# Optimization experiments

Hardware: AMD Instinct MI355X
Metric: run time of the kernel (lower is better)

Reference implementation:

```python
import jax, jax.numpy as jnp
import numpy as np

N, E, G = 20000, 100000, 32
HID, HEADS, HC = 64, 8, 64  # hidden, heads, per-head channels (PyG: out_channels per head)
L, K = 3, 4


def setup_inputs() -> dict:
    key = jax.random.key(0)
    ks = jax.random.split(key, 20)
    rn = lambda k, s, sc=0.05: jax.random.normal(k, s, jnp.float32) * sc
    HO = HEADS * HC  # 512
    return {
        "x": jax.random.uniform(ks[0], (N, 7), jnp.float32),
        "edge_attr": jax.random.normal(ks[1], (E, 4), jnp.float32),
        "means": jax.random.normal(ks[2], (K, 8), jnp.float32),
        "log_stds": jnp.zeros((K, 8), jnp.float32),
        "sp_W": rn(ks[3], (K, HID), 0.3), "sp_b": jnp.zeros((HID,), jnp.float32),
        "ne_W": rn(ks[4], (7, HID), 0.3), "ne_b": jnp.zeros((HID,), jnp.float32),
        "ee_W": rn(ks[5], (4, HID), 0.3), "ee_b": jnp.zeros((HID,), jnp.float32),
        "Wq": rn(ks[6], (L, HID, HO)), "bq": jnp.zeros((L, HO), jnp.float32),
        "Wk": rn(ks[7], (L, HID, HO)), "bk": jnp.zeros((L, HO), jnp.float32),
        "Wv": rn(ks[8], (L, HID, HO)), "bv": jnp.zeros((L, HO), jnp.float32),
        "We": rn(ks[9], (L, HID, HO)), "be": jnp.zeros((L, HO), jnp.float32),
        "Ws": rn(ks[10], (L, HID, HID)), "bs": jnp.zeros((L, HID), jnp.float32),
        "eu_W": rn(ks[11], (L, 3 * HID, HID)), "eu_b": jnp.zeros((L, HID), jnp.float32),
        "rW1": rn(ks[12], (2 * HID, HID)), "rb1": jnp.zeros((HID,), jnp.float32),
        "rW2": rn(ks[13], (HID, HID)), "rb2": jnp.zeros((HID,), jnp.float32),
        "rW3": rn(ks[14], (HID, 2)), "rb3": jnp.zeros((2,), jnp.float32),
        "edge_index": jax.random.randint(ks[15], (2, E), 0, N, jnp.int32),
        "batch": jnp.sort(jax.random.randint(ks[16], (N,), 0, G, jnp.int32)),
        "num_graphs": G,
    }


def reference(x, edge_attr, means, log_stds, sp_W, sp_b, ne_W, ne_b, ee_W, ee_b,
              Wq, bq, Wk, bk, Wv, bv, We, be, Ws, bs, eu_W, eu_b,
              rW1, rb1, rW2, rb2, rW3, rb3, edge_index, batch, num_graphs):
    n = x.shape[0]
    src, dst = edge_index[0], edge_index[1]

    # ---- SpatialGaussianEncoder (dropout is identity in eval) ----
    p = x[:, :4]
    sl, sr = p[src, :2], p[src, 2:4]
    dl, dr = p[dst, :2], p[dst, 2:4]
    rel = jnp.stack([dl - sl, dl - sr, dr - sl, dr - sr], axis=1)  # [E,4,2]
    dist = jnp.linalg.norm(rel, axis=-1)                           # [E,4]
    ang = jnp.arctan2(rel[..., 1], rel[..., 0])                    # [E,4]
    u = jnp.stack([dist, ang], axis=-1).reshape(-1, 8)             # [E,8] (d,a)x4
    std = jnp.exp(log_stds) + 1e-6                                 # [K,8]
    z = (u[:, None, :] - means[None]) / std[None]                  # [E,K,8]
    w = jnp.exp(-0.5 * jnp.sum(z * z, axis=-1))                    # [E,K]
    sp = jax.nn.relu(w @ sp_W + sp_b)                              # [E,HID]

    h = jax.nn.relu(x @ ne_W + ne_b)                               # [N,HID]
    ea = jax.nn.relu(edge_attr @ ee_W + ee_b) + sp                 # [E,HID]

    scale = 1.0 / float(np.sqrt(HC))
    for l in range(L):
        # PyG TransformerConv(hidden, hidden, heads=8, edge_dim=hidden, concat=False)
        q = (h @ Wq[l] + bq[l]).reshape(n, HEADS, HC)
        k = (h @ Wk[l] + bk[l]).reshape(n, HEADS, HC)
        v = (h @ Wv[l] + bv[l]).reshape(n, HEADS, HC)
        e = (ea @ We[l] + be[l]).reshape(-1, HEADS, HC)
        kj = k[src] + e                                            # [E,H,C]
        alpha = jnp.einsum('ehc,ehc->eh', q[dst], kj) * scale      # [E,H]
        m = jax.ops.segment_max(alpha, dst, num_segments=n)
        ex = jnp.exp(alpha - m[dst])
        den = jax.ops.segment_sum(ex, dst, num_segments=n)
        a = ex / (den[dst] + 1e-16)                                # scatter-softmax over dst
        msg = a[:, :, None] * (v[src] + e)                         # [E,H,C]
        out = jax.ops.segment_sum(msg, dst, num_segments=n).mean(axis=1)  # concat=False -> head mean
        h = jax.nn.relu(out + h @ Ws[l] + bs[l])                   # skip (root_weight) + F.relu
        ef = jnp.concatenate([h[src], h[dst], ea], axis=1)         # [E,3*HID]
        ea = jax.nn.relu(ef @ eu_W[l] + eu_b[l])

    # ---- per-graph masked-mean pooling == segment mean ----
    cn = jnp.maximum(jax.ops.segment_sum(jnp.ones((n,), x.dtype), batch, num_segments=num_graphs), 1.0)
    node_pool = jax.ops.segment_sum(h, batch, num_segments=num_graphs) / cn[:, None]
    eb = batch[src]
    ce = jnp.maximum(jax.ops.segment_sum(jnp.ones((src.shape[0],), x.dtype), eb, num_segments=num_graphs), 1.0)
    edge_pool = jax.ops.segment_sum(ea, eb, num_segments=num_graphs) / ce[:, None]
    g = jnp.concatenate([node_pool, edge_pool], axis=1)            # [G,2*HID]

    h1 = jax.nn.relu(g @ rW1 + rb1)
    h2 = jax.nn.relu(h1 @ rW2 + rb2)
    return jnp.tanh(h2 @ rW3 + rb3)                                # [G,2]
```

## Files before the change

### kernel.cpp

```cpp
#include <hip/hip_runtime.h>
#include <hip/hip_bf16.h>
#include <cstdint>
#include <cstddef>



__global__ void __launch_bounds__(256) k_node_embed(
    const float* __restrict__ x, const float* __restrict__ neW, const float* __restrict__ neb,
    float* __restrict__ h, int N)
{
    int idx = blockIdx.x * 256 + threadIdx.x;
    int n = idx >> 6, c = idx & 63;
    if (n >= N) return;
    float acc = neb[c];
    #pragma unroll
    for (int j = 0; j < 7; ++j) acc += x[(size_t)n * 7 + j] * neW[j * 64 + c];
    h[(size_t)n * 64 + c] = fmaxf(acc, 0.f);
}

__global__ void __launch_bounds__(256) k_edge_w(
    const float* __restrict__ x,
    const float* __restrict__ means, const float* __restrict__ log_stds,
    const int* __restrict__ src, const int* __restrict__ dst,
    float* __restrict__ wbuf, int E)
{
    int e = blockIdx.x * 256 + threadIdx.x;
    if (e >= E) return;
    int s = src[e], d = dst[e];
    const float* ps = x + (size_t)s * 7;
    const float* pd = x + (size_t)d * 7;
    float slx = ps[0], sly = ps[1], srx = ps[2], sry = ps[3];
    float dlx = pd[0], dly = pd[1], drx = pd[2], dry = pd[3];
    float u[8];
    float rx, ry;
    rx = dlx - slx; ry = dly - sly; u[0] = sqrtf(rx*rx + ry*ry); u[1] = atan2f(ry, rx);
    rx = dlx - srx; ry = dly - sry; u[2] = sqrtf(rx*rx + ry*ry); u[3] = atan2f(ry, rx);
    rx = drx - slx; ry = dry - sly; u[4] = sqrtf(rx*rx + ry*ry); u[5] = atan2f(ry, rx);
    rx = drx - srx; ry = dry - sry; u[6] = sqrtf(rx*rx + ry*ry); u[7] = atan2f(ry, rx);
    #pragma unroll
    for (int kk = 0; kk < 4; ++kk) {
        float ssum = 0.f;
        #pragma unroll
        for (int dd = 0; dd < 8; ++dd) {
            float stdv = expf(log_stds[kk*8+dd]) + 1e-6f;
            float z = (u[dd] - means[kk*8+dd]) / stdv;
            ssum += z * z;
        }
        wbuf[(size_t)e*4 + kk] = expf(-0.5f * ssum);
    }
}

__global__ void __launch_bounds__(256) k_edge_ea(
    const float* __restrict__ edge_attr, const float* __restrict__ wbuf,
    const float* __restrict__ spW, const float* __restrict__ spb,
    const float* __restrict__ eeW, const float* __restrict__ eeb,
    float* __restrict__ ea, int E)
{
    int idx = blockIdx.x * 256 + threadIdx.x;
    int e = idx >> 6, c = idx & 63;
    if (e >= E) return;
    float acce = eeb[c];
    #pragma unroll
    for (int j = 0; j < 4; ++j) acce += edge_attr[(size_t)e*4 + j] * eeW[j*64 + c];
    float accs = spb[c];
    #pragma unroll
    for (int j = 0; j < 4; ++j) accs += wbuf[(size_t)e*4 + j] * spW[j*64 + c];
    ea[(size_t)e*64 + c] = fmaxf(acce, 0.f) + fmaxf(accs, 0.f);
}


__global__ void __launch_bounds__(256) k_hist(
    const int* __restrict__ dst, int* __restrict__ deg, int E)
{
    int e = blockIdx.x * 256 + threadIdx.x;
    if (e < E) atomicAdd(deg + dst[e], 1);
}

__global__ void __launch_bounds__(1024) k_scan(
    const int* __restrict__ deg, int* __restrict__ ptr, int* __restrict__ headw, int N)
{
    __shared__ int part[1024];
    int t = threadIdx.x;
    int per = (N + 1023) / 1024;
    int s = 0;
    for (int i = 0; i < per; ++i) { int idx = t*per + i; if (idx < N) s += deg[idx]; }
    part[t] = s;
    __syncthreads();
    for (int off = 1; off < 1024; off <<= 1) {
        int v = (t >= off) ? part[t - off] : 0;
        __syncthreads();
        part[t] += v;
        __syncthreads();
    }
    int base = (t > 0) ? part[t - 1] : 0;
    for (int i = 0; i < per; ++i) {
        int idx = t*per + i;
        if (idx < N) { ptr[idx] = base; headw[idx] = base; base += deg[idx]; }
    }
    if (t == 1023) ptr[N] = part[1023];
}

__global__ void __launch_bounds__(256) k_scatter(
    const int* __restrict__ dst, const int* __restrict__ src, const int* __restrict__ batch,
    int* __restrict__ headw, int2* __restrict__ ipair, int* __restrict__ ieb, int E)
{
    int e = blockIdx.x * 256 + threadIdx.x;
    if (e < E) {
        int s = src[e];
        int pos = atomicAdd(headw + dst[e], 1);
        ipair[pos] = make_int2(s, e);
        ieb[e] = batch[s];
    }
}


__global__ void __launch_bounds__(256) k_wprod_all(
    const float* __restrict__ Wq, const float* __restrict__ bq,
    const float* __restrict__ Wk, const float* __restrict__ We,
    float* __restrict__ Mk, float* __restrict__ Me,
    float* __restrict__ bqk, float* __restrict__ bqe)
{
    int h = blockIdx.x;
    int which = blockIdx.y;
    int l = blockIdx.z;
    const float* Wq_l = Wq + (size_t)l * 64 * 512;
    const float* bq_l = bq + (size_t)l * 512;
    const float* Wx_l = (which ? We : Wk) + (size_t)l * 64 * 512;
    float* M  = (which ? Me : Mk) + (size_t)l * 64 * 512;
    float* bM = (which ? bqe : bqk) + (size_t)l * 512;
    __shared__ float wq_s[65][64];
    __shared__ float wx_s[64][65];
    int tid = threadIdx.x;
    for (int i = tid; i < 4096; i += 256) {
        int r = i >> 6, c2 = i & 63;
        wq_s[r][c2] = Wq_l[(size_t)r*512 + h*64 + c2];
        wx_s[r][c2] = Wx_l[(size_t)r*512 + h*64 + c2];
    }
    if (tid < 64) wq_s[64][tid] = bq_l[h*64 + tid];
    __syncthreads();
    int j = tid & 63, cg = tid >> 6;
    for (int c = cg*16; c < cg*16 + 16; ++c) {
        float s = 0.f;
        #pragma unroll 8
        for (int c2 = 0; c2 < 64; ++c2) s += wq_s[c][c2] * wx_s[j][c2];
        M[(size_t)c*512 + h*64 + j] = s;
    }
    if (tid < 64) {
        float s = 0.f;
        #pragma unroll 8
        for (int c2 = 0; c2 < 64; ++c2) s += wq_s[64][c2] * wx_s[tid][c2];
        bM[h*64 + tid] = s;
    }
}

__global__ void __launch_bounds__(64) k_wqb_all(
    const float* __restrict__ Wq, const float* __restrict__ bq,
    const float* __restrict__ bk, const float* __restrict__ be,
    float* __restrict__ wqb, float* __restrict__ cb)
{
    int l = blockIdx.x;
    const float* Wq_l = Wq + (size_t)l * 64 * 512;
    const float* bq_l = bq + (size_t)l * 512;
    const float* bk_l = bk + (size_t)l * 512;
    const float* be_l = be + (size_t)l * 512;
    float* wqb_l = wqb + (size_t)l * 512;
    float* cb_l  = cb + (size_t)l * 8;
    int c = threadIdx.x;
    for (int h = 0; h < 8; ++h) {
        float s = 0.f;
        for (int c2 = 0; c2 < 64; ++c2)
            s += Wq_l[(size_t)c*512 + h*64 + c2] * (bk_l[h*64+c2] + be_l[h*64+c2]);
        wqb_l[c*8 + h] = s;
    }
    if (c < 8) {
        float s = 0.f;
        for (int c2 = 0; c2 < 64; ++c2)
            s += bq_l[c*64 + c2] * (bk_l[c*64+c2] + be_l[c*64+c2]);
        cb_l[c] = s;
    }
}


__global__ void __launch_bounds__(256) k_proj16(
    const float* __restrict__ h,
    const float* __restrict__ Mk, const float* __restrict__ bqk, float* __restrict__ qk,
    const float* __restrict__ Me, const float* __restrict__ bqe, float* __restrict__ qe2,
    int N)
{
    __shared__ float As[64][132];
    __shared__ __align__(16) float Wt[64][64];
    int tid = threadIdx.x;
    int y = blockIdx.y;
    int which = y >> 3, yb = y & 7;
    const float* W    = which ? Me : Mk;
    const float* bias = (which ? bqe : bqk) + yb * 64;
    float* Y          = which ? qe2 : qk;
    int n0 = blockIdx.x * 128;
    {
        int rt = tid & 127;
        int n = n0 + rt;
        int jh = (tid >> 7) * 32;
        if (n < N) {
            const float* ap = h + (size_t)n*64;
            #pragma unroll
            for (int j4 = 0; j4 < 8; ++j4) {
                int j = jh + j4 * 4;
                float4 a = *(const float4*)(ap + j);
                As[j+0][rt] = a.x; As[j+1][rt] = a.y;
                As[j+2][rt] = a.z; As[j+3][rt] = a.w;
            }
        } else {
            #pragma unroll
            for (int j4 = 0; j4 < 8; ++j4) {
                int j = jh + j4 * 4;
                As[j+0][rt] = 0.f; As[j+1][rt] = 0.f;
                As[j+2][rt] = 0.f; As[j+3][rt] = 0.f;
            }
        }
        #pragma unroll
        for (int i = 0; i < 4; ++i) {
            int idx = tid + i * 256;
            int j = idx >> 4, c4 = (idx & 15) * 4;
            *(float4*)&Wt[j][c4] = *(const float4*)(W + (size_t)j*512 + yb*64 + c4);
        }
    }
    __syncthreads();
    int wv = tid >> 6, lane = tid & 63;
    int rg = lane >> 3, cg = lane & 7;
    int c0 = cg * 8;
    int rbase = wv * 32 + rg * 4;
    float acc[4][8];
    float4 b0 = *(const float4*)(bias + c0);
    float4 b1 = *(const float4*)(bias + c0 + 4);
    #pragma unroll
    for (int t = 0; t < 4; ++t) {
        acc[t][0]=b0.x; acc[t][1]=b0.y; acc[t][2]=b0.z; acc[t][3]=b0.w;
        acc[t][4]=b1.x; acc[t][5]=b1.y; acc[t][6]=b1.z; acc[t][7]=b1.w;
    }
    #pragma unroll 4
    for (int j = 0; j < 64; ++j) {
        float4 av = *(const float4*)&As[j][rbase];
        float4 w0 = *(const float4*)&Wt[j][c0];
        float4 w1 = *(const float4*)&Wt[j][c0 + 4];
        acc[0][0] += av.x*w0.x; acc[0][1] += av.x*w0.y; acc[0][2] += av.x*w0.z; acc[0][3] += av.x*w0.w;
        acc[0][4] += av.x*w1.x; acc[0][5] += av.x*w1.y; acc[0][6] += av.x*w1.z; acc[0][7] += av.x*w1.w;
        acc[1][0] += av.y*w0.x; acc[1][1] += av.y*w0.y; acc[1][2] += av.y*w0.z; acc[1][3] += av.y*w0.w;
        acc[1][4] += av.y*w1.x; acc[1][5] += av.y*w1.y; acc[1][6] += av.y*w1.z; acc[1][7] += av.y*w1.w;
        acc[2][0] += av.z*w0.x; acc[2][1] += av.z*w0.y; acc[2][2] += av.z*w0.z; acc[2][3] += av.z*w0.w;
        acc[2][4] += av.z*w1.x; acc[2][5] += av.z*w1.y; acc[2][6] += av.z*w1.z; acc[2][7] += av.z*w1.w;
        acc[3][0] += av.w*w0.x; acc[3][1] += av.w*w0.y; acc[3][2] += av.w*w0.z; acc[3][3] += av.w*w0.w;
        acc[3][4] += av.w*w1.x; acc[3][5] += av.w*w1.y; acc[3][6] += av.w*w1.z; acc[3][7] += av.w*w1.w;
    }
    #pragma unroll
    for (int t = 0; t < 4; ++t) {
        int n = n0 + rbase + t;
        if (n < N) {
            float4 o0 = {acc[t][0],acc[t][1],acc[t][2],acc[t][3]};
            float4 o1 = {acc[t][4],acc[t][5],acc[t][6],acc[t][7]};
            *(float4*)(Y + (size_t)n*512 + yb*64 + c0)     = o0;
            *(float4*)(Y + (size_t)n*512 + yb*64 + c0 + 4) = o1;
        }
    }
}


__global__ void __launch_bounds__(256) k_attn_fused(
    const float* __restrict__ qk, const float* __restrict__ qe2,
    const float* __restrict__ wqb, const float* __restrict__ cb,
    const float* __restrict__ ea, const float* __restrict__ hbuf,
    const int* __restrict__ ptr, const int2* __restrict__ ipair,
    float* __restrict__ hagg, float* __restrict__ tbuf, float* __restrict__ sbuf, int N)
{
    int wv = threadIdx.x >> 6, lane = threadIdx.x & 63;
    int n = blockIdx.x * 4 + wv;
    if (n >= N) return;
    int h = lane >> 3, p = lane & 7;
    int b = ptr[n], e_ = ptr[n + 1];
    int deg = e_ - b;
    const float4* xp = (const float4*)(qk + (size_t)n*512 + lane*8);
    float4 x0 = xp[0], x1 = xp[1];
    const float4* gp = (const float4*)(qe2 + (size_t)n*512 + lane*8);
    float4 g0 = gp[0], g1 = gp[1];
    const float4* hdp = (const float4*)(hbuf + (size_t)n*64 + p*8);
    float4 hd0 = hdp[0], hd1 = hdp[1];
    float qbh = hd0.x*wqb[(p*8+0)*8+h] + hd0.y*wqb[(p*8+1)*8+h]
              + hd0.z*wqb[(p*8+2)*8+h] + hd0.w*wqb[(p*8+3)*8+h]
              + hd1.x*wqb[(p*8+4)*8+h] + hd1.y*wqb[(p*8+5)*8+h]
              + hd1.z*wqb[(p*8+6)*8+h] + hd1.w*wqb[(p*8+7)*8+h];
    qbh += __shfl_xor(qbh, 1);
    qbh += __shfl_xor(qbh, 2);
    qbh += __shfl_xor(qbh, 4);
    qbh += cb[h];
    float m = -3.4e38f, den = 0.f;
    float hacc[8], tacc[8];
    #pragma unroll
    for (int i = 0; i < 8; ++i) { hacc[i] = 0.f; tacc[i] = 0.f; }
    for (int base = 0; base < deg; base += 64) {
        int cnt = deg - base; if (cnt > 64) cnt = 64;
        int2 myp = (lane < cnt) ? ipair[b + base + lane] : make_int2(0, 0);
        int s0i = __shfl(myp.x, 0), e0i = __shfl(myp.y, 0);
        const float4* hp = (const float4*)(hbuf + (size_t)s0i*64 + p*8);
        const float4* ap = (const float4*)(ea + (size_t)e0i*64 + p*8);
        float4 h0 = hp[0], h1 = hp[1];
        float4 a0 = ap[0], a1 = ap[1];
        for (int i = 0; i < cnt; ++i) {
            float4 h0c = h0, h1c = h1, a0c = a0, a1c = a1;
            if (i + 1 < cnt) {
                int sn = __shfl(myp.x, i + 1), en = __shfl(myp.y, i + 1);
                const float4* hpn = (const float4*)(hbuf + (size_t)sn*64 + p*8);
                const float4* apn = (const float4*)(ea + (size_t)en*64 + p*8);
                h0 = hpn[0]; h1 = hpn[1]; a0 = apn[0]; a1 = apn[1];
            }
            float t = x0.x*h0c.x + x0.y*h0c.y + x0.z*h0c.z + x0.w*h0c.w
                    + x1.x*h1c.x + x1.y*h1c.y + x1.z*h1c.z + x1.w*h1c.w
                    + g0.x*a0c.x + g0.y*a0c.y + g0.z*a0c.z + g0.w*a0c.w
                    + g1.x*a1c.x + g1.y*a1c.y + g1.z*a1c.z + g1.w*a1c.w;
            t += __shfl_xor(t, 1);
            t += __shfl_xor(t, 2);
            t += __shfl_xor(t, 4);
            float al = 0.125f * (t + qbh);
            float mn = fmaxf(m, al);
            float r = expf(m - mn);
            float w = expf(al - mn);
            den = den * r + w;
            m = mn;
            hacc[0] = hacc[0]*r + w*h0c.x; hacc[1] = hacc[1]*r + w*h0c.y;
            hacc[2] = hacc[2]*r + w*h0c.z; hacc[3] = hacc[3]*r + w*h0c.w;
            hacc[4] = hacc[4]*r + w*h1c.x; hacc[5] = hacc[5]*r + w*h1c.y;
            hacc[6] = hacc[6]*r + w*h1c.z; hacc[7] = hacc[7]*r + w*h1c.w;
            tacc[0] = tacc[0]*r + w*a0c.x; tacc[1] = tacc[1]*r + w*a0c.y;
            tacc[2] = tacc[2]*r + w*a0c.z; tacc[3] = tacc[3]*r + w*a0c.w;
            tacc[4] = tacc[4]*r + w*a1c.x; tacc[5] = tacc[5]*r + w*a1c.y;
            tacc[6] = tacc[6]*r + w*a1c.z; tacc[7] = tacc[7]*r + w*a1c.w;
        }
    }
    float inv = 0.125f / (den + 1e-16f);
    float4 o;
    o = {hacc[0]*inv,hacc[1]*inv,hacc[2]*inv,hacc[3]*inv};
    *(float4*)(hagg + (size_t)n*512 + lane*8)     = o;
    o = {hacc[4]*inv,hacc[5]*inv,hacc[6]*inv,hacc[7]*inv};
    *(float4*)(hagg + (size_t)n*512 + lane*8 + 4) = o;
    o = {tacc[0]*inv,tacc[1]*inv,tacc[2]*inv,tacc[3]*inv};
    *(float4*)(tbuf + (size_t)n*512 + lane*8)     = o;
    o = {tacc[4]*inv,tacc[5]*inv,tacc[6]*inv,tacc[7]*inv};
    *(float4*)(tbuf + (size_t)n*512 + lane*8 + 4) = o;
    if (p == 0) sbuf[(size_t)n*8 + h] = den * inv;
}

__global__ void __launch_bounds__(256) k_nf_gemm2(
    const float* __restrict__ tbuf, const float* __restrict__ hagg,
    const float* __restrict__ We, const float* __restrict__ Wv,
    float* __restrict__ pbuf, int N)
{
    __shared__ float As[64][132];
    __shared__ __align__(16) float Wt[64][64];
    int tid = threadIdx.x;
    int g = blockIdx.y;
    int n0 = blockIdx.x * 128;
    int wv = tid >> 6, lane = tid & 63;
    int rg = lane >> 3, cg = lane & 7;
    int c0 = cg * 8;
    int rbase = wv * 32 + rg * 4;
    float acc[4][8];
    #pragma unroll
    for (int t = 0; t < 4; ++t)
        #pragma unroll
        for (int i = 0; i < 8; ++i) acc[t][i] = 0.f;
    #pragma unroll
    for (int yy = 0; yy < 2; ++yy) {
        int y = g * 2 + yy;
        #pragma unroll
        for (int round = 0; round < 2; ++round) {
            const float* A = round ? hagg : tbuf;
            const float* W = round ? Wv : We;
            {
                int rt = tid & 127;
                int n = n0 + rt;
                int jh = (tid >> 7) * 32;
                if (n < N) {
                    const float* ap = A + (size_t)n*512 + y*64;
                    #pragma unroll
                    for (int j4 = 0; j4 < 8; ++j4) {
                        int j = jh + j4 * 4;
                        float4 a = *(const float4*)(ap + j);
                        As[j+0][rt] = a.x; As[j+1][rt] = a.y;
                        As[j+2][rt] = a.z; As[j+3][rt] = a.w;
                    }
                } else {
                    #pragma unroll
                    for (int j4 = 0; j4 < 8; ++j4) {
                        int j = jh + j4 * 4;
                        As[j+0][rt] = 0.f; As[j+1][rt] = 0.f;
                        As[j+2][rt] = 0.f; As[j+3][rt] = 0.f;
                    }
                }
                #pragma unroll
                for (int i = 0; i < 4; ++i) {
                    int idx = tid + i * 256;
                    int j = idx >> 4, c4 = (idx & 15) * 4;
                    *(float4*)&Wt[j][c4] = *(const float4*)(W + (size_t)j*512 + y*64 + c4);
                }
            }
            __syncthreads();
            #pragma unroll 4
            for (int j = 0; j < 64; ++j) {
                float4 av = *(const float4*)&As[j][rbase];
                float4 w0 = *(const float4*)&Wt[j][c0];
                float4 w1 = *(const float4*)&Wt[j][c0 + 4];
                acc[0][0] += av.x*w0.x; acc[0][1] += av.x*w0.y; acc[0][2] += av.x*w0.z; acc[0][3] += av.x*w0.w;
                acc[0][4] += av.x*w1.x; acc[0][5] += av.x*w1.y; acc[0][6] += av.x*w1.z; acc[0][7] += av.x*w1.w;
                acc[1][0] += av.y*w0.x; acc[1][1] += av.y*w0.y; acc[1][2] += av.y*w0.z; acc[1][3] += av.y*w0.w;
                acc[1][4] += av.y*w1.x; acc[1][5] += av.y*w1.y; acc[1][6] += av.y*w1.z; acc[1][7] += av.y*w1.w;
                acc[2][0] += av.z*w0.x; acc[2][1] += av.z*w0.y; acc[2][2] += av.z*w0.z; acc[2][3] += av.z*w0.w;
                acc[2][4] += av.z*w1.x; acc[2][5] += av.z*w1.y; acc[2][6] += av.z*w1.z; acc[2][7] += av.z*w1.w;
                acc[3][0] += av.w*w0.x; acc[3][1] += av.w*w0.y; acc[3][2] += av.w*w0.z; acc[3][3] += av.w*w0.w;
                acc[3][4] += av.w*w1.x; acc[3][5] += av.w*w1.y; acc[3][6] += av.w*w1.z; acc[3][7] += av.w*w1.w;
            }
            __syncthreads();
        }
    }
    float* out = pbuf + (size_t)g * N * 64;
    #pragma unroll
    for (int t = 0; t < 4; ++t) {
        int n = n0 + rbase + t;
        if (n < N) {
            float4 o0 = {acc[t][0],acc[t][1],acc[t][2],acc[t][3]};
            float4 o1 = {acc[t][4],acc[t][5],acc[t][6],acc[t][7]};
            *(float4*)(out + (size_t)n*64 + c0)     = o0;
            *(float4*)(out + (size_t)n*64 + c0 + 4) = o1;
        }
    }
}

__global__ void __launch_bounds__(256) k_nf_reduce2(
    const float* __restrict__ pbuf, const float* __restrict__ hin,
    const float* __restrict__ sbuf, const float* __restrict__ Ws,
    const float* __restrict__ be, const float* __restrict__ bv,
    const float* __restrict__ bs, float* __restrict__ hnext, int N)
{
    int idx = blockIdx.x * 256 + threadIdx.x;
    int n = idx >> 6, cc = idx & 63;
    if (n >= N) return;
    float a = bs[cc];
    #pragma unroll
    for (int y = 0; y < 4; ++y) a += pbuf[(size_t)y*N*64 + (size_t)n*64 + cc];
    float hv = hin[(size_t)n*64 + cc];
    #pragma unroll 8
    for (int j = 0; j < 64; ++j) a += __shfl(hv, j) * Ws[(size_t)j*64 + cc];
    #pragma unroll
    for (int h = 0; h < 8; ++h)
        a += sbuf[(size_t)n*8 + h] * (be[h*64 + cc] + bv[h*64 + cc]);
    hnext[(size_t)n*64 + cc] = fmaxf(a, 0.f);
}

__global__ void __launch_bounds__(256) k_eu_pre(
    const float* __restrict__ h, const float* __restrict__ euW,
    float* __restrict__ hw, int N)
{
    __shared__ float As[64][132];
    __shared__ __align__(16) float Wt[64][64];
    int tid = threadIdx.x;
    int y = blockIdx.y;
    int n0 = blockIdx.x * 128;
    {
        int rt = tid & 127;
        int n = n0 + rt;
        int jh = (tid >> 7) * 32;
        if (n < N) {
            const float* ap = h + (size_t)n*64;
            #pragma unroll
            for (int j4 = 0; j4 < 8; ++j4) {
                int j = jh + j4 * 4;
                float4 a = *(const float4*)(ap + j);
                As[j+0][rt] = a.x; As[j+1][rt] = a.y;
                As[j+2][rt] = a.z; As[j+3][rt] = a.w;
            }
        } else {
            #pragma unroll
            for (int j4 = 0; j4 < 8; ++j4) {
                int j = jh + j4 * 4;
                As[j+0][rt] = 0.f; As[j+1][rt] = 0.f;
                As[j+2][rt] = 0.f; As[j+3][rt] = 0.f;
            }
        }
        #pragma unroll
        for (int i = 0; i < 4; ++i) {
            int idx = tid + i * 256;
            *(float4*)&Wt[idx >> 4][(idx & 15) * 4] =
                *(const float4*)(euW + (size_t)y*4096 + idx * 4);
        }
    }
    __syncthreads();
    int wv = tid >> 6, lane = tid & 63;
    int rg = lane >> 3, cg = lane & 7;
    int c0 = cg * 8;
    int rbase = wv * 32 + rg * 4;
    float acc[4][8];
    #pragma unroll
    for (int t = 0; t < 4; ++t)
        #pragma unroll
        for (int i = 0; i < 8; ++i) acc[t][i] = 0.f;
    #pragma unroll 4
    for (int j = 0; j < 64; ++j) {
        float4 av = *(const float4*)&As[j][rbase];
        float4 w0 = *(const float4*)&Wt[j][c0];
        float4 w1 = *(const float4*)&Wt[j][c0 + 4];
        acc[0][0] += av.x*w0.x; acc[0][1] += av.x*w0.y; acc[0][2] += av.x*w0.z; acc[0][3] += av.x*w0.w;
        acc[0][4] += av.x*w1.x; acc[0][5] += av.x*w1.y; acc[0][6] += av.x*w1.z; acc[0][7] += av.x*w1.w;
        acc[1][0] += av.y*w0.x; acc[1][1] += av.y*w0.y; acc[1][2] += av.y*w0.z; acc[1][3] += av.y*w0.w;
        acc[1][4] += av.y*w1.x; acc[1][5] += av.y*w1.y; acc[1][6] += av.y*w1.z; acc[1][7] += av.y*w1.w;
        acc[2][0] += av.z*w0.x; acc[2][1] += av.z*w0.y; acc[2][2] += av.z*w0.z; acc[2][3] += av.z*w0.w;
        acc[2][4] += av.z*w1.x; acc[2][5] += av.z*w1.y; acc[2][6] += av.z*w1.z; acc[2][7] += av.z*w1.w;
        acc[3][0] += av.w*w0.x; acc[3][1] += av.w*w0.y; acc[3][2] += av.w*w0.z; acc[3][3] += av.w*w0.w;
        acc[3][4] += av.w*w1.x; acc[3][5] += av.w*w1.y; acc[3][6] += av.w*w1.z; acc[3][7] += av.w*w1.w;
    }
    #pragma unroll
    for (int t = 0; t < 4; ++t) {
        int n = n0 + rbase + t;
        if (n < N) {
            float4 o0 = {acc[t][0],acc[t][1],acc[t][2],acc[t][3]};
            float4 o1 = {acc[t][4],acc[t][5],acc[t][6],acc[t][7]};
            *(float4*)(hw + (size_t)n*128 + y*64 + c0)     = o0;
            *(float4*)(hw + (size_t)n*128 + y*64 + c0 + 4) = o1;
        }
    }
}

__global__ void __launch_bounds__(256) k_edge_update2(
    const float* __restrict__ hw, const float* __restrict__ ea,
    const float* __restrict__ euW2, const float* __restrict__ eub,
    const int* __restrict__ src, const int* __restrict__ dst,
    float* __restrict__ ea2, int E)
{
    __shared__ float As[64][132];
    __shared__ __align__(16) float Wt[64][64];
    __shared__ int sid[128], did[128];
    int tid = threadIdx.x;
    int e0 = blockIdx.x * 128;
    if (tid < 128) {
        int e = e0 + tid; if (e >= E) e = E - 1;
        sid[tid] = src[e]; did[tid] = dst[e];
    }
    {
        int et = tid & 127;
        int e = e0 + et; if (e >= E) e = E - 1;
        const float* ap = ea + (size_t)e * 64;
        int jh = (tid >> 7) * 32;
        #pragma unroll
        for (int j4 = 0; j4 < 8; ++j4) {
            int j = jh + j4 * 4;
            float4 a = *(const float4*)(ap + j);
            As[j+0][et] = a.x; As[j+1][et] = a.y;
            As[j+2][et] = a.z; As[j+3][et] = a.w;
        }
        #pragma unroll
        for (int i = 0; i < 4; ++i) {
            int idx = tid + i * 256;
            *(float4*)&Wt[idx >> 4][(idx & 15) * 4] = *(const float4*)(euW2 + idx * 4);
        }
    }
    __syncthreads();
    int wv = tid >> 6, lane = tid & 63;
    int rg = lane >> 3, cg = lane & 7;
    int c0 = cg * 8;
    int rbase = wv * 32 + rg * 4;
    float acc[4][8];
    float4 b0 = *(const float4*)(eub + c0);
    float4 b1 = *(const float4*)(eub + c0 + 4);
    #pragma unroll
    for (int t = 0; t < 4; ++t) {
        acc[t][0]=b0.x; acc[t][1]=b0.y; acc[t][2]=b0.z; acc[t][3]=b0.w;
        acc[t][4]=b1.x; acc[t][5]=b1.y; acc[t][6]=b1.z; acc[t][7]=b1.w;
    }
    #pragma unroll 4
    for (int j = 0; j < 64; ++j) {
        float4 av = *(const float4*)&As[j][rbase];
        float4 w0 = *(const float4*)&Wt[j][c0];
        float4 w1 = *(const float4*)&Wt[j][c0 + 4];
        acc[0][0] += av.x*w0.x; acc[0][1] += av.x*w0.y; acc[0][2] += av.x*w0.z; acc[0][3] += av.x*w0.w;
        acc[0][4] += av.x*w1.x; acc[0][5] += av.x*w1.y; acc[0][6] += av.x*w1.z; acc[0][7] += av.x*w1.w;
        acc[1][0] += av.y*w0.x; acc[1][1] += av.y*w0.y; acc[1][2] += av.y*w0.z; acc[1][3] += av.y*w0.w;
        acc[1][4] += av.y*w1.x; acc[1][5] += av.y*w1.y; acc[1][6] += av.y*w1.z; acc[1][7] += av.y*w1.w;
        acc[2][0] += av.z*w0.x; acc[2][1] += av.z*w0.y; acc[2][2] += av.z*w0.z; acc[2][3] += av.z*w0.w;
        acc[2][4] += av.z*w1.x; acc[2][5] += av.z*w1.y; acc[2][6] += av.z*w1.z; acc[2][7] += av.z*w1.w;
        acc[3][0] += av.w*w0.x; acc[3][1] += av.w*w0.y; acc[3][2] += av.w*w0.z; acc[3][3] += av.w*w0.w;
        acc[3][4] += av.w*w1.x; acc[3][5] += av.w*w1.y; acc[3][6] += av.w*w1.z; acc[3][7] += av.w*w1.w;
    }
    #pragma unroll
    for (int t = 0; t < 4; ++t) {
        int e = e0 + rbase + t;
        if (e < E) {
            int s = sid[rbase + t], d = did[rbase + t];
            const float4* sp = (const float4*)(hw + (size_t)s*128 + c0);
            const float4* dp = (const float4*)(hw + (size_t)d*128 + 64 + c0);
            float4 s0 = sp[0], s1 = sp[1];
            float4 d0 = dp[0], d1 = dp[1];
            float4 o0 = {fmaxf(acc[t][0]+s0.x+d0.x,0.f), fmaxf(acc[t][1]+s0.y+d0.y,0.f),
                         fmaxf(acc[t][2]+s0.z+d0.z,0.f), fmaxf(acc[t][3]+s0.w+d0.w,0.f)};
            float4 o1 = {fmaxf(acc[t][4]+s1.x+d1.x,0.f), fmaxf(acc[t][5]+s1.y+d1.y,0.f),
                         fmaxf(acc[t][6]+s1.z+d1.z,0.f), fmaxf(acc[t][7]+s1.w+d1.w,0.f)};
            *(float4*)(ea2 + (size_t)e*64 + c0)     = o0;
            *(float4*)(ea2 + (size_t)e*64 + c0 + 4) = o1;
        }
    }
}


__global__ void __launch_bounds__(64) k_node_pool(
    const float* __restrict__ h, const int* __restrict__ batch,
    float* __restrict__ npool, float* __restrict__ cn, int N)
{
    int lane = threadIdx.x;
    int n0 = blockIdx.x * 64;
    float acc = 0.f; int cur = -1; int run = 0;
    for (int i = 0; i < 64; ++i) {
        int n = n0 + i;
        if (n >= N) break;
        int b = batch[n];
        if (b != cur) {
            if (cur >= 0) {
                atomicAdd(npool + (size_t)cur*64 + lane, acc);
                if (lane == 0) atomicAdd(cn + cur, (float)run);
            }
            cur = b; acc = 0.f; run = 0;
        }
        acc += h[(size_t)n*64 + lane];
        ++run;
    }
    if (cur >= 0) {
        atomicAdd(npool + (size_t)cur*64 + lane, acc);
        if (lane == 0) atomicAdd(cn + cur, (float)run);
    }
}

__global__ void __launch_bounds__(256) k_edge_pool2(
    const float* __restrict__ ea, const int* __restrict__ ieb,
    float* __restrict__ rep, int E)
{
    __shared__ float pool_s[32][64];
    __shared__ float cnt_s[32];
    int tid = threadIdx.x;
    for (int i = tid; i < 2048; i += 256) ((float*)pool_s)[i] = 0.f;
    if (tid < 32) cnt_s[tid] = 0.f;
    __syncthreads();
    int wv = tid >> 6, lane = tid & 63;
    int base = blockIdx.x * 64 + wv * 16;
    int b16[16]; float v16[16];
    #pragma unroll
    for (int u = 0; u < 16; ++u) {
        int e = base + u;
        bool ok = (e < E);
        b16[u] = ok ? ieb[e] : -1;
        v16[u] = ok ? ea[(size_t)e*64 + lane] : 0.f;
    }
    #pragma unroll
    for (int u = 0; u < 16; ++u) {
        if (b16[u] >= 0) {
            atomicAdd(&pool_s[b16[u]][lane], v16[u]);
            if (lane == 0) atomicAdd(&cnt_s[b16[u]], 1.f);
        }
    }
    __syncthreads();
    float* myrep = rep + (size_t)(blockIdx.x & 7) * 2080;
    for (int i = tid; i < 2048; i += 256) atomicAdd(myrep + i, ((float*)pool_s)[i]);
    if (tid < 32) atomicAdd(myrep + 2048 + tid, cnt_s[tid]);
}

__global__ void __launch_bounds__(256) k_pool_merge(
    const float* __restrict__ rep, float* __restrict__ epool, float* __restrict__ ce)
{
    int i = blockIdx.x * 256 + threadIdx.x;
    if (i < 2080) {
        float s = 0.f;
        #pragma unroll
        for (int r = 0; r < 8; ++r) s += rep[(size_t)r*2080 + i];
        if (i < 2048) epool[i] = s; else ce[i - 2048] = s;
    }
}

__global__ void __launch_bounds__(64) k_head_mlp(
    const float* __restrict__ npool, const float* __restrict__ epool,
    const float* __restrict__ cn, const float* __restrict__ ce,
    const float* __restrict__ rW1, const float* __restrict__ rb1,
    const float* __restrict__ rW2, const float* __restrict__ rb2,
    const float* __restrict__ rW3, const float* __restrict__ rb3,
    float* __restrict__ out)
{
    __shared__ float g[128];
    __shared__ float h1[64];
    __shared__ float h2[64];
    int b = blockIdx.x, lane = threadIdx.x;
    float cnv = fmaxf(cn[b], 1.f), cev = fmaxf(ce[b], 1.f);
    g[lane]      = npool[(size_t)b*64 + lane] / cnv;
    g[64 + lane] = epool[(size_t)b*64 + lane] / cev;
    __syncthreads();
    float acc = rb1[lane];
    #pragma unroll 4
    for (int j = 0; j < 128; ++j) acc += g[j] * rW1[j*64 + lane];
    h1[lane] = fmaxf(acc, 0.f);
    __syncthreads();
    acc = rb2[lane];
    #pragma unroll 4
    for (int j = 0; j < 64; ++j) acc += h1[j] * rW2[j*64 + lane];
    h2[lane] = fmaxf(acc, 0.f);
    __syncthreads();
    if (lane < 2) {
        float o = rb3[lane];
        for (int j = 0; j < 64; ++j) o += h2[j] * rW3[j*2 + lane];
        out[b*2 + lane] = tanhf(o);
    }
}


extern "C" void kernel_launch(void* const* d_in, const int* in_sizes, int n_in,
                              void* d_out, int out_size, void* d_ws, size_t ws_size,
                              hipStream_t stream)
{
    const float* x         = (const float*)d_in[0];
    const float* edge_attr = (const float*)d_in[1];
    const float* means     = (const float*)d_in[2];
    const float* log_stds  = (const float*)d_in[3];
    const float* spW       = (const float*)d_in[4];
    const float* spb       = (const float*)d_in[5];
    const float* neW       = (const float*)d_in[6];
    const float* neb       = (const float*)d_in[7];
    const float* eeW       = (const float*)d_in[8];
    const float* eeb       = (const float*)d_in[9];
    const float* Wq        = (const float*)d_in[10];
    const float* bq        = (const float*)d_in[11];
    const float* Wk        = (const float*)d_in[12];
    const float* bk        = (const float*)d_in[13];
    const float* Wv        = (const float*)d_in[14];
    const float* bv        = (const float*)d_in[15];
    const float* We        = (const float*)d_in[16];
    const float* be        = (const float*)d_in[17];
    const float* Ws        = (const float*)d_in[18];
    const float* bs        = (const float*)d_in[19];
    const float* euW       = (const float*)d_in[20];
    const float* eub       = (const float*)d_in[21];
    const float* rW1       = (const float*)d_in[22];
    const float* rb1       = (const float*)d_in[23];
    const float* rW2       = (const float*)d_in[24];
    const float* rb2       = (const float*)d_in[25];
    const float* rW3       = (const float*)d_in[26];
    const float* rb3       = (const float*)d_in[27];
    const int* eidx        = (const int*)d_in[28];
    const int* batch       = (const int*)d_in[29];

    int N = in_sizes[0] / 7;
    int E = in_sizes[1] / 4;
    const int G = 32;
    const int* srcp = eidx;
    const int* dstp = eidx + E;

    float* ws = (float*)d_ws;
    size_t fl = 0;
    float* hA    = ws + fl; fl += (size_t)N * 64;
    float* hB    = ws + fl; fl += (size_t)N * 64;
    float* eaA   = ws + fl; fl += (size_t)E * 64;
    float* eaB   = ws + fl; fl += (size_t)E * 64;
    float* B1    = ws + fl; fl += (size_t)N * 512;
    float* B2    = ws + fl; fl += (size_t)N * 512;
    float* B3    = ws + fl; fl += (size_t)N * 512;
    float* alpha = ws + fl; fl += (size_t)E * 8;
    float* sbuf  = ws + fl; fl += (size_t)N * 8;
    float* npool = ws + fl; fl += (size_t)G * 64;
    float* epool = ws + fl; fl += (size_t)G * 64;
    float* cn    = ws + fl; fl += G;
    float* ce    = ws + fl; fl += G;
    float* Mk3   = ws + fl; fl += 3 * 64 * 512;
    float* Me3   = ws + fl; fl += 3 * 64 * 512;
    float* bqk3  = ws + fl; fl += 3 * 512;
    float* bqe3  = ws + fl; fl += 3 * 512;
    float* wqb3  = ws + fl; fl += 3 * 512;
    float* cb3   = ws + fl; fl += 24;
    float* rep   = ws + fl; fl += 8 * 2080;
    int* ideg  = (int*)(ws + fl); fl += (size_t)N;
    int* ihead = (int*)(ws + fl); fl += (size_t)N;
    int2* ipair = (int2*)(ws + fl); fl += (size_t)E * 2;
    int* ieb   = (int*)(ws + fl); fl += (size_t)E;
    int* iptr  = (int*)(ws + fl); fl += (size_t)N + 1;

    float* wbuf = alpha;

    hipMemsetAsync(npool, 0, (size_t)(G * 130) * sizeof(float), stream);
    hipMemsetAsync(rep, 0, (size_t)(8 * 2080) * sizeof(float), stream);
    hipMemsetAsync(ideg, 0, (size_t)N * sizeof(int), stream);

    k_node_embed<<<(N * 64 + 255) / 256, 256, 0, stream>>>(x, neW, neb, hA, N);
    k_edge_w<<<(E + 255) / 256, 256, 0, stream>>>(x, means, log_stds, srcp, dstp, wbuf, E);
    k_edge_ea<<<((size_t)E * 64 + 255) / 256, 256, 0, stream>>>(edge_attr, wbuf,
                                                                spW, spb, eeW, eeb, eaA, E);
    k_hist<<<(E + 255) / 256, 256, 0, stream>>>(dstp, ideg, E);
    k_scan<<<1, 1024, 0, stream>>>(ideg, iptr, ihead, N);
    k_scatter<<<(E + 255) / 256, 256, 0, stream>>>(dstp, srcp, batch, ihead, ipair, ieb, E);
    k_wprod_all<<<dim3(8, 2, 3), 256, 0, stream>>>(Wq, bq, Wk, We, Mk3, Me3, bqk3, bqe3);
    k_wqb_all<<<3, 64, 0, stream>>>(Wq, bq, bk, be, wqb3, cb3);

    float* hcur = hA;  float* hnext = hB;
    float* eacur = eaA; float* eanext = eaB;
    for (int l = 0; l < 3; ++l) {
        const float* Wv_l = Wv + (size_t)l * 64 * 512;
        const float* We_l = We + (size_t)l * 64 * 512;
        const float* bv_l = bv + (size_t)l * 512;
        const float* be_l = be + (size_t)l * 512;
        const float* euW_l = euW + (size_t)l * 192 * 64;

        k_proj16<<<dim3((N + 127) / 128, 16), 256, 0, stream>>>(
            hcur,
            Mk3 + (size_t)l * 32768, bqk3 + (size_t)l * 512, B1,
            Me3 + (size_t)l * 32768, bqe3 + (size_t)l * 512, B2, N);

        k_attn_fused<<<(N + 3) / 4, 256, 0, stream>>>(B1, B2,
                                                      wqb3 + (size_t)l * 512,
                                                      cb3 + (size_t)l * 8,
                                                      eacur, hcur,
                                                      iptr, ipair,
                                                      B1 , B2 , sbuf, N);
        k_nf_gemm2<<<dim3((N + 127) / 128, 4), 256, 0, stream>>>(B2, B1, We_l, Wv_l, B3, N);
        k_nf_reduce2<<<((size_t)N * 64 + 255) / 256, 256, 0, stream>>>(B3, hcur, sbuf,
                                                                       Ws + (size_t)l * 64 * 64,
                                                                       be_l, bv_l,
                                                                       bs + (size_t)l * 64,
                                                                       hnext, N);
        k_eu_pre<<<dim3((N + 127) / 128, 2), 256, 0, stream>>>(hnext, euW_l, B3, N);
        k_edge_update2<<<(E + 127) / 128, 256, 0, stream>>>(B3, eacur, euW_l + 2 * 4096,
                                                            eub + (size_t)l * 64,
                                                            srcp, dstp, eanext, E);
        float* t1 = hcur; hcur = hnext; hnext = t1;
        float* t2 = eacur; eacur = eanext; eanext = t2;
    }

    k_node_pool<<<(N + 63) / 64, 64, 0, stream>>>(hcur, batch, npool, cn, N);
    k_edge_pool2<<<(E + 63) / 64, 256, 0, stream>>>(eacur, ieb, rep, E);
    k_pool_merge<<<9, 256, 0, stream>>>(rep, epool, ce);
    k_head_mlp<<<G, 64, 0, stream>>>(npool, epool, cn, ce, rW1, rb1, rW2, rb2, rW3, rb3,
                                     (float*)d_out);
}
```

Measured before the change: 732.5 us.

## Split nf_gemm2 per head and prefetch second operand into registers

The per-head GEMM kernel now handles one head per block (8 y-blocks instead of 4 blocks covering 2 heads each), and the partial-sum reduce sums 8 partials instead of 4. Inside the kernel, the hagg and Wv tiles for the second round are loaded into registers before the first round's compute, so their global latency overlaps with that compute. This doubles the block count for more parallelism, but it also doubles the partial buffer written and read by the reduce kernel, which costs extra memory traffic and needs a larger scratch buffer.

```diff
diff --git a/kernel.cpp b/kernel.cpp
--- a/kernel.cpp
+++ b/kernel.cpp
@@ -355,8 +355,54 @@
     __shared__ float As[64][132];
     __shared__ __align__(16) float Wt[64][64];
     int tid = threadIdx.x;
-    int g = blockIdx.y;
+    int y = blockIdx.y;
     int n0 = blockIdx.x * 128;
+    int rt = tid & 127;
+    int jh = (tid >> 7) * 32;
+    int nrow = n0 + rt;
+    bool rowok = (nrow < N);
+    {
+        if (rowok) {
+            const float* ap = tbuf + (size_t)nrow*512 + y*64;
+            #pragma unroll
+            for (int j4 = 0; j4 < 8; ++j4) {
+                int j = jh + j4 * 4;
+                float4 a = *(const float4*)(ap + j);
+                As[j+0][rt] = a.x; As[j+1][rt] = a.y;
+                As[j+2][rt] = a.z; As[j+3][rt] = a.w;
+            }
+        } else {
+            #pragma unroll
+            for (int j4 = 0; j4 < 8; ++j4) {
+                int j = jh + j4 * 4;
+                As[j+0][rt] = 0.f; As[j+1][rt] = 0.f;
+                As[j+2][rt] = 0.f; As[j+3][rt] = 0.f;
+            }
+        }
+        #pragma unroll
+        for (int i = 0; i < 4; ++i) {
+            int idx = tid + i * 256;
+            int j = idx >> 4, c4 = (idx & 15) * 4;
+            *(float4*)&Wt[j][c4] = *(const float4*)(We + (size_t)j*512 + y*64 + c4);
+        }
+    }
+    __syncthreads();
+    float4 pa[8];
+    float4 pw[4];
+    if (rowok) {
+        const float* ap2 = hagg + (size_t)nrow*512 + y*64;
+        #pragma unroll
+        for (int j4 = 0; j4 < 8; ++j4) pa[j4] = *(const float4*)(ap2 + jh + j4*4);
+    } else {
+        #pragma unroll
+        for (int j4 = 0; j4 < 8; ++j4) pa[j4] = make_float4(0.f, 0.f, 0.f, 0.f);
+    }
+    #pragma unroll
+    for (int i = 0; i < 4; ++i) {
+        int idx = tid + i * 256;
+        int j = idx >> 4, c4 = (idx & 15) * 4;
+        pw[i] = *(const float4*)(Wv + (size_t)j*512 + y*64 + c4);
+    }
     int wv = tid >> 6, lane = tid & 63;
     int rg = lane >> 3, cg = lane & 7;
     int c0 = cg * 8;
@@ -366,60 +412,49 @@
     for (int t = 0; t < 4; ++t)
         #pragma unroll
         for (int i = 0; i < 8; ++i) acc[t][i] = 0.f;
-    #pragma unroll
-    for (int yy = 0; yy < 2; ++yy) {
-        int y = g * 2 + yy;
-        #pragma unroll
-        for (int round = 0; round < 2; ++round) {
-            const float* A = round ? hagg : tbuf;
-            const float* W = round ? Wv : We;
-            {
-                int rt = tid & 127;
-                int n = n0 + rt;
-                int jh = (tid >> 7) * 32;
-                if (n < N) {
-                    const float* ap = A + (size_t)n*512 + y*64;
-                    #pragma unroll
-                    for (int j4 = 0; j4 < 8; ++j4) {
-                        int j = jh + j4 * 4;
-                        float4 a = *(const float4*)(ap + j);
-                        As[j+0][rt] = a.x; As[j+1][rt] = a.y;
-                        As[j+2][rt] = a.z; As[j+3][rt] = a.w;
-                    }
-                } else {
-                    #pragma unroll
-                    for (int j4 = 0; j4 < 8; ++j4) {
-                        int j = jh + j4 * 4;
-                        As[j+0][rt] = 0.f; As[j+1][rt] = 0.f;
-                        As[j+2][rt] = 0.f; As[j+3][rt] = 0.f;
-                    }
-                }
-                #pragma unroll
-                for (int i = 0; i < 4; ++i) {
-                    int idx = tid + i * 256;
-                    int j = idx >> 4, c4 = (idx & 15) * 4;
-                    *(float4*)&Wt[j][c4] = *(const float4*)(W + (size_t)j*512 + y*64 + c4);
-                }
-            }
-            __syncthreads();
-            #pragma unroll 4
-            for (int j = 0; j < 64; ++j) {
-                float4 av = *(const float4*)&As[j][rbase];
-                float4 w0 = *(const float4*)&Wt[j][c0];
-                float4 w1 = *(const float4*)&Wt[j][c0 + 4];
-                acc[0][0] += av.x*w0.x; acc[0][1] += av.x*w0.y; acc[0][2] += av.x*w0.z; acc[0][3] += av.x*w0.w;
-                acc[0][4] += av.x*w1.x; acc[0][5] += av.x*w1.y; acc[0][6] += av.x*w1.z; acc[0][7] += av.x*w1.w;
-                acc[1][0] += av.y*w0.x; acc[1][1] += av.y*w0.y; acc[1][2] += av.y*w0.z; acc[1][3] += av.y*w0.w;
-                acc[1][4] += av.y*w1.x; acc[1][5] += av.y*w1.y; acc[1][6] += av.y*w1.z; acc[1][7] += av.y*w1.w;
-                acc[2][0] += av.z*w0.x; acc[2][1] += av.z*w0.y; acc[2][2] += av.z*w0.z; acc[2][3] += av.z*w0.w;
-                acc[2][4] += av.z*w1.x; acc[2][5] += av.z*w1.y; acc[2][6] += av.z*w1.z; acc[2][7] += av.z*w1.w;
-                acc[3][0] += av.w*w0.x; acc[3][1] += av.w*w0.y; acc[3][2] += av.w*w0.z; acc[3][3] += av.w*w0.w;
-                acc[3][4] += av.w*w1.x; acc[3][5] += av.w*w1.y; acc[3][6] += av.w*w1.z; acc[3][7] += av.w*w1.w;
-            }
-            __syncthreads();
-        }
-    }
-    float* out = pbuf + (size_t)g * N * 64;
+    #pragma unroll 4
+    for (int j = 0; j < 64; ++j) {
+        float4 av = *(const float4*)&As[j][rbase];
+        float4 w0 = *(const float4*)&Wt[j][c0];
+        float4 w1 = *(const float4*)&Wt[j][c0 + 4];
+        acc[0][0] += av.x*w0.x; acc[0][1] += av.x*w0.y; acc[0][2] += av.x*w0.z; acc[0][3] += av.x*w0.w;
+        acc[0][4] += av.x*w1.x; acc[0][5] += av.x*w1.y; acc[0][6] += av.x*w1.z; acc[0][7] += av.x*w1.w;
+        acc[1][0] += av.y*w0.x; acc[1][1] += av.y*w0.y; acc[1][2] += av.y*w0.z; acc[1][3] += av.y*w0.w;
+        acc[1][4] += av.y*w1.x; acc[1][5] += av.y*w1.y; acc[1][6] += av.y*w1.z; acc[1][7] += av.y*w1.w;
+        acc[2][0] += av.z*w0.x; acc[2][1] += av.z*w0.y; acc[2][2] += av.z*w0.z; acc[2][3] += av.z*w0.w;
+        acc[2][4] += av.z*w1.x; acc[2][5] += av.z*w1.y; acc[2][6] += av.z*w1.z; acc[2][7] += av.z*w1.w;
+        acc[3][0] += av.w*w0.x; acc[3][1] += av.w*w0.y; acc[3][2] += av.w*w0.z; acc[3][3] += av.w*w0.w;
+        acc[3][4] += av.w*w1.x; acc[3][5] += av.w*w1.y; acc[3][6] += av.w*w1.z; acc[3][7] += av.w*w1.w;
+    }
+    __syncthreads();
+    #pragma unroll
+    for (int j4 = 0; j4 < 8; ++j4) {
+        int j = jh + j4 * 4;
+        As[j+0][rt] = pa[j4].x; As[j+1][rt] = pa[j4].y;
+        As[j+2][rt] = pa[j4].z; As[j+3][rt] = pa[j4].w;
+    }
+    #pragma unroll
+    for (int i = 0; i < 4; ++i) {
+        int idx = tid + i * 256;
+        int j = idx >> 4, c4 = (idx & 15) * 4;
+        *(float4*)&Wt[j][c4] = pw[i];
+    }
+    __syncthreads();
+    #pragma unroll 4
+    for (int j = 0; j < 64; ++j) {
+        float4 av = *(const float4*)&As[j][rbase];
+        float4 w0 = *(const float4*)&Wt[j][c0];
+        float4 w1 = *(const float4*)&Wt[j][c0 + 4];
+        acc[0][0] += av.x*w0.x; acc[0][1] += av.x*w0.y; acc[0][2] += av.x*w0.z; acc[0][3] += av.x*w0.w;
+        acc[0][4] += av.x*w1.x; acc[0][5] += av.x*w1.y; acc[0][6] += av.x*w1.z; acc[0][7] += av.x*w1.w;
+        acc[1][0] += av.y*w0.x; acc[1][1] += av.y*w0.y; acc[1][2] += av.y*w0.z; acc[1][3] += av.y*w0.w;
+        acc[1][4] += av.y*w1.x; acc[1][5] += av.y*w1.y; acc[1][6] += av.y*w1.z; acc[1][7] += av.y*w1.w;
+        acc[2][0] += av.z*w0.x; acc[2][1] += av.z*w0.y; acc[2][2] += av.z*w0.z; acc[2][3] += av.z*w0.w;
+        acc[2][4] += av.z*w1.x; acc[2][5] += av.z*w1.y; acc[2][6] += av.z*w1.z; acc[2][7] += av.z*w1.w;
+        acc[3][0] += av.w*w0.x; acc[3][1] += av.w*w0.y; acc[3][2] += av.w*w0.z; acc[3][3] += av.w*w0.w;
+        acc[3][4] += av.w*w1.x; acc[3][5] += av.w*w1.y; acc[3][6] += av.w*w1.z; acc[3][7] += av.w*w1.w;
+    }
+    float* out = pbuf + (size_t)y * N * 64;
     #pragma unroll
     for (int t = 0; t < 4; ++t) {
         int n = n0 + rbase + t;
@@ -443,7 +478,7 @@
     if (n >= N) return;
     float a = bs[cc];
     #pragma unroll
-    for (int y = 0; y < 4; ++y) a += pbuf[(size_t)y*N*64 + (size_t)n*64 + cc];
+    for (int y = 0; y < 8; ++y) a += pbuf[(size_t)y*N*64 + (size_t)n*64 + cc];
     float hv = hin[(size_t)n*64 + cc];
     #pragma unroll 8
     for (int j = 0; j < 64; ++j) a += __shfl(hv, j) * Ws[(size_t)j*64 + cc];
@@ -817,7 +852,7 @@
                                                       eacur, hcur,
                                                       iptr, ipair,
                                                       B1 , B2 , sbuf, N);
-        k_nf_gemm2<<<dim3((N + 127) / 128, 4), 256, 0, stream>>>(B2, B1, We_l, Wv_l, B3, N);
+        k_nf_gemm2<<<dim3((N + 127) / 128, 8), 256, 0, stream>>>(B2, B1, We_l, Wv_l, B3, N);
         k_nf_reduce2<<<((size_t)N * 64 + 255) / 256, 256, 0, stream>>>(B3, hcur, sbuf,
                                                                        Ws + (size_t)l * 64 * 64,
                                                                        be_l, bv_l,
```

New measurement: 727.7 us. Within noise of the previous version (-0.7%).
